# Optimization experiments

Measured on AMD Instinct MI355X. Metric: run time of the kernel, lower is better.

## Reference

```python
import jax, jax.numpy as jnp
import numpy as np

DIM = 1024
HEAD_DIM = 64
CHUNK = 128
B, T = 4, 4096


def setup_inputs() -> dict:
    key = jax.random.key(0)
    ks = jax.random.split(key, 8)
    s = 1.0 / np.sqrt(DIM)
    inp = {
        'x': jax.random.normal(ks[0], (B, T, DIM), jnp.float32),
        'Wq': jax.random.normal(ks[1], (DIM, DIM), jnp.float32) * s,
        'bq': jnp.zeros((DIM,), jnp.float32),
        'Wk': jax.random.normal(ks[2], (DIM, DIM), jnp.float32) * s,
        'bk': jnp.zeros((DIM,), jnp.float32),
        'Wv': jax.random.normal(ks[3], (DIM, DIM), jnp.float32) * s,
        'bv': jnp.zeros((DIM,), jnp.float32),
        'Wbeta': jax.random.normal(ks[4], (DIM, DIM), jnp.float32) * s,
        'bbeta': jnp.zeros((DIM,), jnp.float32),
        'Walpha': jax.random.normal(ks[5], (DIM, DIM), jnp.float32) * s,
        'balpha': jnp.full((DIM,), 2.0, jnp.float32),  # bias init 2.0 as in torch
    }
    return inp


def reference(x, Wq, bq, Wk, bk, Wv, bv, Wbeta, bbeta, Walpha, balpha):
    Bsz, Tlen, D = x.shape
    d = HEAD_DIM
    H = D // d
    C = CHUNK
    scale = d ** (-0.5)

    q = ((x @ Wq.T + bq) * scale).reshape(Bsz, Tlen, H, d)
    k = ((x @ Wk.T + bk) * scale).reshape(Bsz, Tlen, H, d)
    v = (x @ Wv.T + bv).reshape(Bsz, Tlen, H, d)
    alpha_logits = jnp.clip((x @ Walpha.T + balpha).reshape(Bsz, Tlen, H, d), -10.0, 10.0)
    log_alpha = jax.nn.log_sigmoid(alpha_logits)
    alpha_val = jax.nn.sigmoid(alpha_logits)
    beta = jax.nn.softplus(x @ Wbeta.T + bbeta).reshape(Bsz, Tlen, H, d)

    # pad T to a multiple of C (static)
    pad = (-Tlen) % C
    if pad:
        pw = ((0, 0), (0, pad), (0, 0), (0, 0))
        q, k, v = jnp.pad(q, pw), jnp.pad(k, pw), jnp.pad(v, pw)
        log_alpha, beta = jnp.pad(log_alpha, pw), jnp.pad(beta, pw)
    N = q.shape[1] // C
    cshape = (Bsz, N, C, H, d)
    q, k, v = q.reshape(cshape), k.reshape(cshape), v.reshape(cshape)
    log_alpha, beta = log_alpha.reshape(cshape), beta.reshape(cshape)

    ccum = jnp.cumsum(log_alpha, axis=2)          # (B,N,C,H,d)
    m = ccum.mean(axis=-1)                        # (B,N,C,H); mean is linear -> take before pairwise diff
    decay_logits_mean = m[:, :, :, None, :] - m[:, :, None, :, :]  # (B,N,C,C,H)
    tril = jnp.tril(jnp.ones((C, C), jnp.float32))[None, None, :, :, None]
    decay_logits_mean = jnp.where(tril == 0, -1e9, decay_logits_mean)
    decay = jnp.exp(decay_logits_mean)            # (B,N,C,C,H)

    attn = jnp.einsum('bnihd,bnjhd->bnhij', q, k)
    attn = attn * decay.transpose(0, 1, 4, 2, 3)
    y_intra = jnp.einsum('bnhij,bnjhd->bnihd', attn, v * beta)  # (B,N,C,H,d)

    # inter-chunk recurrence via scan over chunks
    asum = jnp.exp(log_alpha.sum(axis=2).mean(axis=-1))  # (B,N,H) total chunk decay
    curve = jnp.exp(m)                                   # (B,N,C,H) intra-chunk decay curve
    bmean = beta.mean(axis=-1)                           # (B,N,C,H)

    def to_scan(a):
        return jnp.moveaxis(a, 1, 0)
    xs = (to_scan(q), to_scan(y_intra), to_scan(curve), to_scan(asum),
          to_scan(k), to_scan(v), to_scan(bmean))

    state0 = jnp.zeros((Bsz, H, d, d), jnp.float32)

    def step(state, inputs):
        qi, yi, ci, ai, ki, vi, bmi = inputs
        mem = jnp.einsum('bchq,bhqk->bchk', qi, state)
        y = yi + mem * ci[..., None]
        state = state * ai[:, :, None, None]
        delta = jnp.einsum('bchk,bchv,bch->bhkv', ki, vi, bmi)
        return state + delta, y

    state, ys = jax.lax.scan(step, state0, xs)
    y = jnp.moveaxis(ys, 0, 1).reshape(Bsz, N * C, D)
    if pad:
        y = y[:, :Tlen, :]
    return y, state, alpha_val
```

## Files before the change

### kernel.cpp

```cpp
#include <hip/hip_runtime.h>
#include <cstdint>
#include <cmath>

#define DIMM 1024
#define NHEAD 16
#define HEADD 64
#define CHUNKC 128
#define NBATCH 4
#define TLEN 4096
#define NCHUNK 32
#define BT (NBATCH * TLEN)
#define NSTACK (5 * DIMM)

typedef unsigned short ushort_t;
typedef __attribute__((ext_vector_type(8))) short short8;
typedef __attribute__((ext_vector_type(4))) float f32x4;

__device__ __forceinline__ float blo(unsigned int u) { return __uint_as_float(u << 16); }
__device__ __forceinline__ float bhi(unsigned int u) { return __uint_as_float(u & 0xffff0000u); }
__device__ __forceinline__ ushort_t f2bf(float f) {
  unsigned int u = __float_as_uint(f);
  u += 0x7fffu + ((u >> 16) & 1u);
  return (ushort_t)(u >> 16);
}
__device__ __forceinline__ float bf2f(ushort_t s) { return __uint_as_float(((unsigned int)s) << 16); }
__device__ __forceinline__ unsigned pack2(float a, float b) {
  return (unsigned)f2bf(a) | ((unsigned)f2bf(b) << 16);
}

__device__ __forceinline__ void async16(const ushort_t* g, ushort_t* l) {
  __builtin_amdgcn_global_load_lds((__attribute__((address_space(1))) void*)g,
                                   (__attribute__((address_space(3))) void*)l, 16, 0, 0);
}

__global__ __launch_bounds__(256) void k_cast(
    const float* __restrict__ x,
    const float* __restrict__ Wq, const float* __restrict__ Wk,
    const float* __restrict__ Wv, const float* __restrict__ Wb, const float* __restrict__ Wa,
    const float* __restrict__ bq, const float* __restrict__ bk,
    const float* __restrict__ bv, const float* __restrict__ bb, const float* __restrict__ ba,
    ushort_t* __restrict__ xb, ushort_t* __restrict__ wbm, float* __restrict__ bias_st) {
  const long XU = (long)BT * DIMM / 4;
  const long WU = (long)NSTACK * DIMM / 4;
  const long BU = NSTACK / 4;
  const long NU = XU + WU + BU;
  for (long u = (long)blockIdx.x * blockDim.x + threadIdx.x; u < NU;
       u += (long)gridDim.x * blockDim.x) {
    if (u < XU) {
      float4 f = ((const float4*)x)[u];
      ushort4 o;
      o.x = f2bf(f.x); o.y = f2bf(f.y); o.z = f2bf(f.z); o.w = f2bf(f.w);
      ((ushort4*)xb)[u] = o;
    } else if (u < XU + WU) {
      long j = u - XU;
      long e = j * 4;
      int row = (int)(e >> 10);
      int col = (int)(e & 1023);
      int p = row >> 10, wr = row & 1023;
      const float* Wp = (p == 0) ? Wq : (p == 1) ? Wk : (p == 2) ? Wv : (p == 3) ? Wb : Wa;
      float4 f = *(const float4*)(Wp + (size_t)wr * DIMM + col);
      ushort4 o;
      o.x = f2bf(f.x); o.y = f2bf(f.y); o.z = f2bf(f.z); o.w = f2bf(f.w);
      ((ushort4*)wbm)[j] = o;
    } else {
      long j = u - XU - WU;
      int e = (int)(j * 4);
      int p = e >> 10, r = e & 1023;
      const float* bp = (p == 0) ? bq : (p == 1) ? bk : (p == 2) ? bv : (p == 3) ? bb : ba;
      ((float4*)bias_st)[j] = *(const float4*)(bp + r);
    }
  }
}

__global__ __launch_bounds__(256) void k_proj(
    const ushort_t* __restrict__ xb, const ushort_t* __restrict__ wbm,
    const float* __restrict__ bias_st,
    ushort_t* __restrict__ qo, ushort_t* __restrict__ ko,
    ushort_t* __restrict__ vo, ushort_t* __restrict__ bo,
    float* __restrict__ ao) {
  __shared__ ushort_t As[128 * 32];
  __shared__ ushort_t Bs[128 * 32];
  const int tid = threadIdx.x;
  const int bn0 = blockIdx.x * 128;
  const int bm0 = blockIdx.y * 128;
  const int lane = tid & 63;
  const int wave = tid >> 6;
  const int quad = lane >> 4, lr = lane & 15;
  const int wr = (wave >> 1) * 64, wc = (wave & 1) * 64;

  f32x4 zero = {0.f, 0.f, 0.f, 0.f};
  f32x4 acc[4][4];
#pragma unroll
  for (int i = 0; i < 4; ++i)
#pragma unroll
    for (int j = 0; j < 4; ++j) acc[i][j] = zero;

  const int r0 = tid >> 2;
  const int c0 = (tid & 3) * 8;
  const ushort_t* ag0 = xb + (size_t)(bm0 + r0) * DIMM + c0;
  const ushort_t* ag1 = xb + (size_t)(bm0 + r0 + 64) * DIMM + c0;
  const ushort_t* bg0 = wbm + (size_t)(bn0 + r0) * DIMM + c0;
  const ushort_t* bg1 = wbm + (size_t)(bn0 + r0 + 64) * DIMM + c0;
  ushort_t* la0 = As + tid * 8;
  ushort_t* la1 = As + 2048 + tid * 8;
  ushort_t* lb0 = Bs + tid * 8;
  ushort_t* lb1 = Bs + 2048 + tid * 8;

  for (int kk = 0; kk < DIMM; kk += 32) {
    __syncthreads();
    async16(ag0 + kk, la0);
    async16(ag1 + kk, la1);
    async16(bg0 + kk, lb0);
    async16(bg1 + kk, lb1);
    __syncthreads();
    short8 af[4], bfr[4];
#pragma unroll
    for (int i = 0; i < 4; ++i)
      af[i] = *(const short8*)(As + (wr + i * 16 + lr) * 32 + quad * 8);
#pragma unroll
    for (int j = 0; j < 4; ++j)
      bfr[j] = *(const short8*)(Bs + (wc + j * 16 + lr) * 32 + quad * 8);
#pragma unroll
    for (int i = 0; i < 4; ++i)
#pragma unroll
      for (int j = 0; j < 4; ++j)
        acc[i][j] = __builtin_amdgcn_mfma_f32_16x16x32_bf16(af[i], bfr[j], acc[i][j], 0, 0, 0);
  }

  const int p = bn0 >> 10;
  const int ncol0 = bn0 & 1023;
#pragma unroll
  for (int j = 0; j < 4; ++j) {
    const int colg = wc + j * 16 + lr;
    const float bias = bias_st[bn0 + colg];
    const int nc = ncol0 + colg;
#pragma unroll
    for (int i = 0; i < 4; ++i) {
#pragma unroll
      for (int r = 0; r < 4; ++r) {
        const int rowl = wr + i * 16 + quad * 4 + r;
        const size_t o = (size_t)(bm0 + rowl) * DIMM + nc;
        float val = acc[i][j][r] + bias;
        if (p == 0) {
          qo[o] = f2bf(val * 0.125f);
        } else if (p == 1) {
          ko[o] = f2bf(val * 0.125f);
        } else if (p == 2) {
          vo[o] = f2bf(val);
        } else if (p == 3) {
          float sp = (val > 20.f) ? val : log1pf(expf(val));
          bo[o] = f2bf(sp);
        } else {
          float c = fminf(fmaxf(val, -10.f), 10.f);
          ao[o] = 1.f / (1.f + expf(-c));
        }
      }
    }
  }
}

__global__ __launch_bounds__(128) void k_stats(
    const float* __restrict__ alpha, const ushort_t* __restrict__ betaw,
    float* __restrict__ mArr, float* __restrict__ bmean, float* __restrict__ asum) {
  const int bnh = blockIdx.x;
  const int h = bnh & 15, n = (bnh >> 4) & 31, b = bnh >> 9;
  const int c = threadIdx.x;
  const size_t bt = (size_t)b * TLEN + n * CHUNKC + c;

  const float4* ap = (const float4*)(alpha + bt * DIMM + h * HEADD);
  float ls = 0.f;
#pragma unroll
  for (int w = 0; w < 16; ++w) {
    float4 a = ap[w];
    ls += logf(a.x) + logf(a.y) + logf(a.z) + logf(a.w);
  }
  const uint4* bp = (const uint4*)(betaw + bt * DIMM + h * HEADD);
  float bs = 0.f;
#pragma unroll
  for (int w = 0; w < 8; ++w) {
    uint4 u = bp[w];
    bs += blo(u.x) + bhi(u.x) + blo(u.y) + bhi(u.y) + blo(u.z) + bhi(u.z) + blo(u.w) + bhi(u.w);
  }
  float la = ls * (1.f / 64.f);

  __shared__ float s[128];
  s[c] = la;
  __syncthreads();
  for (int off = 1; off < 128; off <<= 1) {
    float t = (c >= off) ? s[c - off] : 0.f;
    __syncthreads();
    s[c] += t;
    __syncthreads();
  }
  float m = s[c];
  const size_t o = (size_t)bnh * CHUNKC + c;
  mArr[o] = m;
  bmean[o] = bs * (1.f / 64.f);
  if (c == 127) asum[bnh] = expf(m);
}

__global__ __launch_bounds__(256) void k_delta(
    const ushort_t* __restrict__ kw, const ushort_t* __restrict__ vw,
    const float* __restrict__ bmean, float* __restrict__ delta) {
  __shared__ ushort_t kc[8192];
  __shared__ ushort_t vc[8192];
  __shared__ float bm[128];
  const int bnh = blockIdx.x;
  const int h = bnh & 15, n = (bnh >> 4) & 31, b = bnh >> 9;
  const int tid = threadIdx.x;
  const size_t bt0 = (size_t)b * TLEN + n * CHUNKC;

#pragma unroll
  for (int it = 0; it < 4; ++it) {
    int u = tid + it * 256;
    int row = u >> 3, col = (u & 7) * 8;
    size_t go = (bt0 + row) * DIMM + h * HEADD + col;
    ((uint4*)kc)[u] = *(const uint4*)(kw + go);
    ((uint4*)vc)[u] = *(const uint4*)(vw + go);
  }
  if (tid < 128) bm[tid] = bmean[(size_t)bnh * CHUNKC + tid];
  __syncthreads();

  const int kd = tid >> 2, v0 = (tid & 3) * 16;
  float acc[16];
#pragma unroll
  for (int l = 0; l < 16; ++l) acc[l] = 0.f;

#pragma unroll 4
  for (int c = 0; c < 128; ++c) {
    float kb = bf2f(kc[c * 64 + kd]) * bm[c];
    const uint4* vr = (const uint4*)(vc + c * 64 + v0);
    uint4 u0 = vr[0], u1 = vr[1];
    acc[0] += kb * blo(u0.x);  acc[1] += kb * bhi(u0.x);
    acc[2] += kb * blo(u0.y);  acc[3] += kb * bhi(u0.y);
    acc[4] += kb * blo(u0.z);  acc[5] += kb * bhi(u0.z);
    acc[6] += kb * blo(u0.w);  acc[7] += kb * bhi(u0.w);
    acc[8] += kb * blo(u1.x);  acc[9] += kb * bhi(u1.x);
    acc[10] += kb * blo(u1.y); acc[11] += kb * bhi(u1.y);
    acc[12] += kb * blo(u1.z); acc[13] += kb * bhi(u1.z);
    acc[14] += kb * blo(u1.w); acc[15] += kb * bhi(u1.w);
  }
  float* dst = delta + (size_t)bnh * 4096 + kd * 64 + v0;
#pragma unroll
  for (int l4 = 0; l4 < 4; ++l4)
    ((float4*)dst)[l4] = make_float4(acc[l4 * 4], acc[l4 * 4 + 1], acc[l4 * 4 + 2], acc[l4 * 4 + 3]);
}

__global__ __launch_bounds__(256) void k_scan(
    const float* __restrict__ delta, const float* __restrict__ asum,
    float* __restrict__ Earr, float* __restrict__ state_out) {
  const int bh = blockIdx.x >> 4;
  const int g = blockIdx.x & 15;
  const int b = bh >> 4, h = bh & 15;
  const int elem = g * 256 + threadIdx.x;
  float e = 0.f;
  for (int n = 0; n < 32; ++n) {
    const size_t o = (((size_t)b * 32 + n) * 16 + h) * 4096 + elem;
    const float a = asum[((size_t)b * 32 + n) * 16 + h];
    Earr[o] = e;
    e = e * a + delta[o];
  }
  state_out[(size_t)bh * 4096 + elem] = e;
}

__global__ __launch_bounds__(256) void k_y(
    const ushort_t* __restrict__ qw, const ushort_t* __restrict__ kw,
    const ushort_t* __restrict__ vw, const ushort_t* __restrict__ betaw,
    const float* __restrict__ mArr, const float* __restrict__ Earr,
    float* __restrict__ yout) {
  __shared__ __align__(16) ushort_t vbt[64][200];
  __shared__ __align__(16) ushort_t pst[4][32][40];
  __shared__ float ms[128];
  const int bnh = blockIdx.x;
  const int h = bnh & 15, n = (bnh >> 4) & 31, b = bnh >> 9;
  const int tid = threadIdx.x;
  const int lane = tid & 63;
  const int wv = tid >> 6;
  const int quad = lane >> 4, lr = lane & 15;
  const int i0 = wv * 32;
  const size_t bt0 = (size_t)b * TLEN + n * CHUNKC;
  const size_t hoff = (size_t)h * HEADD;

#pragma unroll
  for (int it = 0; it < 4; ++it) {
    int u = tid + it * 256;
    int j = u & 127, vd0 = (u >> 7) * 8;
    size_t go = (bt0 + j) * DIMM + hoff + vd0;
    uint4 vv = *(const uint4*)(vw + go);
    uint4 bb2 = *(const uint4*)(betaw + go);
    vbt[vd0 + 0][j] = f2bf(blo(vv.x) * blo(bb2.x));
    vbt[vd0 + 1][j] = f2bf(bhi(vv.x) * bhi(bb2.x));
    vbt[vd0 + 2][j] = f2bf(blo(vv.y) * blo(bb2.y));
    vbt[vd0 + 3][j] = f2bf(bhi(vv.y) * bhi(bb2.y));
    vbt[vd0 + 4][j] = f2bf(blo(vv.z) * blo(bb2.z));
    vbt[vd0 + 5][j] = f2bf(bhi(vv.z) * bhi(bb2.z));
    vbt[vd0 + 6][j] = f2bf(blo(vv.w) * blo(bb2.w));
    vbt[vd0 + 7][j] = f2bf(bhi(vv.w) * bhi(bb2.w));
  }
  const float4* Eg = (const float4*)(Earr + (size_t)bnh * 4096);
#pragma unroll
  for (int it = 0; it < 4; ++it) {
    int u = tid + it * 256;
    int kd = u >> 4, vd0 = (u & 15) * 4;
    float4 ev = Eg[u];
    vbt[vd0 + 0][128 + kd] = f2bf(ev.x);
    vbt[vd0 + 1][128 + kd] = f2bf(ev.y);
    vbt[vd0 + 2][128 + kd] = f2bf(ev.z);
    vbt[vd0 + 3][128 + kd] = f2bf(ev.w);
  }
  if (tid < 128) ms[tid] = mArr[(size_t)bnh * CHUNKC + tid];
  __syncthreads();

  short8 qa[2][2];
#pragma unroll
  for (int it = 0; it < 2; ++it) {
    const ushort_t* qg = qw + (bt0 + i0 + it * 16 + lr) * DIMM + hoff + quad * 8;
    qa[it][0] = *(const short8*)(qg);
    qa[it][1] = *(const short8*)(qg + 32);
  }
  float mi[2][4];
#pragma unroll
  for (int it = 0; it < 2; ++it)
#pragma unroll
    for (int r = 0; r < 4; ++r) mi[it][r] = ms[i0 + it * 16 + quad * 4 + r];

  f32x4 zero = {0.f, 0.f, 0.f, 0.f};
  f32x4 acc2[2][4];
#pragma unroll
  for (int it = 0; it < 2; ++it)
#pragma unroll
    for (int nt = 0; nt < 4; ++nt) acc2[it][nt] = zero;

  for (int js = 0; js < 4; ++js) {
    const int j0 = js * 32;
#pragma unroll
    for (int jsub = 0; jsub < 2; ++jsub) {
      const int j0s = j0 + jsub * 16;
      const ushort_t* kg = kw + (bt0 + j0s + lr) * DIMM + hoff + quad * 8;
      short8 kb0 = *(const short8*)(kg);
      short8 kb1 = *(const short8*)(kg + 32);
      const float mj = ms[j0s + lr];
#pragma unroll
      for (int it = 0; it < 2; ++it) {
        f32x4 s = __builtin_amdgcn_mfma_f32_16x16x32_bf16(qa[it][0], kb0, zero, 0, 0, 0);
        s = __builtin_amdgcn_mfma_f32_16x16x32_bf16(qa[it][1], kb1, s, 0, 0, 0);
#pragma unroll
        for (int r = 0; r < 4; ++r) {
          const int ig = i0 + it * 16 + quad * 4 + r;
          const int jg = j0s + lr;
          float w = (jg > ig) ? 0.f : s[r] * __expf(mi[it][r] - mj);
          pst[wv][it * 16 + quad * 4 + r][jsub * 16 + lr] = f2bf(w);
        }
      }
    }
#pragma unroll
    for (int it = 0; it < 2; ++it) {
      short8 pa = *(const short8*)&pst[wv][it * 16 + lr][quad * 8];
#pragma unroll
      for (int nt = 0; nt < 4; ++nt) {
        short8 vb = *(const short8*)&vbt[nt * 16 + lr][j0 + quad * 8];
        acc2[it][nt] = __builtin_amdgcn_mfma_f32_16x16x32_bf16(pa, vb, acc2[it][nt], 0, 0, 0);
      }
    }
  }

#pragma unroll
  for (int es = 0; es < 2; ++es) {
    const int kd0 = es * 32;
    {
      const int row = lane >> 1;
      const int col0 = (lane & 1) * 16;
      const float ex = __expf(ms[i0 + row]);
      const ushort_t* qg = qw + (bt0 + i0 + row) * DIMM + hoff + kd0 + col0;
      uint4 u0 = *(const uint4*)(qg);
      uint4 u1 = *(const uint4*)(qg + 8);
      uint4 w0, w1;
      w0.x = pack2(blo(u0.x) * ex, bhi(u0.x) * ex);
      w0.y = pack2(blo(u0.y) * ex, bhi(u0.y) * ex);
      w0.z = pack2(blo(u0.z) * ex, bhi(u0.z) * ex);
      w0.w = pack2(blo(u0.w) * ex, bhi(u0.w) * ex);
      w1.x = pack2(blo(u1.x) * ex, bhi(u1.x) * ex);
      w1.y = pack2(blo(u1.y) * ex, bhi(u1.y) * ex);
      w1.z = pack2(blo(u1.z) * ex, bhi(u1.z) * ex);
      w1.w = pack2(blo(u1.w) * ex, bhi(u1.w) * ex);
      *(uint4*)&pst[wv][row][col0] = w0;
      *(uint4*)&pst[wv][row][col0 + 8] = w1;
    }
#pragma unroll
    for (int it = 0; it < 2; ++it) {
      short8 pa = *(const short8*)&pst[wv][it * 16 + lr][quad * 8];
#pragma unroll
      for (int nt = 0; nt < 4; ++nt) {
        short8 vb = *(const short8*)&vbt[nt * 16 + lr][128 + kd0 + quad * 8];
        acc2[it][nt] = __builtin_amdgcn_mfma_f32_16x16x32_bf16(pa, vb, acc2[it][nt], 0, 0, 0);
      }
    }
  }

#pragma unroll
  for (int it = 0; it < 2; ++it) {
#pragma unroll
    for (int nt = 0; nt < 4; ++nt) {
      f32x4 a = acc2[it][nt];
#pragma unroll
      for (int r = 0; r < 4; ++r) {
        const int ig = i0 + it * 16 + quad * 4 + r;
        yout[(bt0 + ig) * DIMM + hoff + nt * 16 + lr] = a[r];
      }
    }
  }
}

extern "C" void kernel_launch(void* const* d_in, const int* in_sizes, int n_in,
                              void* d_out, int out_size, void* d_ws, size_t ws_size,
                              hipStream_t stream) {
  const float* x  = (const float*)d_in[0];
  const float* Wq = (const float*)d_in[1];
  const float* bq = (const float*)d_in[2];
  const float* Wk = (const float*)d_in[3];
  const float* bk = (const float*)d_in[4];
  const float* Wv = (const float*)d_in[5];
  const float* bv = (const float*)d_in[6];
  const float* Wb = (const float*)d_in[7];
  const float* bb = (const float*)d_in[8];
  const float* Wa = (const float*)d_in[9];
  const float* ba = (const float*)d_in[10];

  char* ws = (char*)d_ws;
  ushort_t* xb   = (ushort_t*)(ws + 0);
  ushort_t* wbm  = (ushort_t*)(ws + 33554432);
  float* bias_st = (float*)(ws + 44040192);
  ushort_t* qw   = (ushort_t*)(ws + 44060672);
  ushort_t* kw   = (ushort_t*)(ws + 77615104);
  ushort_t* vw   = (ushort_t*)(ws + 111169536);
  ushort_t* bw   = (ushort_t*)(ws + 144723968);
  float* mArr    = (float*)(ws + 178278400);
  float* bmean   = (float*)(ws + 179326976);
  float* asum    = (float*)(ws + 180375552);
  float* delta   = (float*)(ws + 180383744);
  float* Earr    = (float*)(ws + 213938176);

  float* yout = (float*)d_out;
  float* state_out = yout + (size_t)BT * DIMM;
  float* aout = state_out + (size_t)NBATCH * NHEAD * 64 * 64;

  k_cast<<<dim3(4096), dim3(256), 0, stream>>>(x, Wq, Wk, Wv, Wb, Wa,
                                               bq, bk, bv, bb, ba, xb, wbm, bias_st);
  k_proj<<<dim3(40, 128), dim3(256), 0, stream>>>(xb, wbm, bias_st, qw, kw, vw, bw, aout);
  k_stats<<<dim3(2048), dim3(128), 0, stream>>>(aout, bw, mArr, bmean, asum);
  k_delta<<<dim3(2048), dim3(256), 0, stream>>>(kw, vw, bmean, delta);
  k_scan<<<dim3(1024), dim3(256), 0, stream>>>(delta, asum, Earr, state_out);
  k_y<<<dim3(2048), dim3(256), 0, stream>>>(qw, kw, vw, bw, mArr, Earr, yout);
}
```

Measured before the change: 661.4 us.

## Rewrite projection GEMM as 256x256 double-buffered ping-pong MFMA pipeline

The fused 5-way projection GEMM moves from 128x128 tiles with K=32 and a full sync per step to 256x256 tiles with K=64, 512 threads and 128KB of double-buffered LDS. Loads are XOR-swizzled to avoid bank conflicts, and async global-to-LDS copies are interleaved with quadrant MFMA blocks using setprio and vmcnt waits. The block index is remapped so neighbouring blocks share tiles in L2. This targets low MFMA utilisation and exposed load latency in the dominant GEMM, but raises register and LDS pressure, and the hand-scheduled barrier ordering is fragile.

Measured after the change: 743.3 us. +12.4%, slower.

```diff
diff --git a/kernel.cpp b/kernel.cpp
--- a/kernel.cpp
+++ b/kernel.cpp
@@ -72,92 +72,149 @@
   }
 }
 
-__global__ __launch_bounds__(256) void k_proj(
+#define REGN(bb,op,hh) ((((bb)*2+(op))*2+(hh))*16384)
+
+#define STAGE(bb,op,hh,kt) do {                                                   \
+    const ushort_t* _g = ((op) ? wbm + (((size_t)(bn0 + (hh)*128 + srow)) << 10)  \
+                               : xb  + (((size_t)(bm0 + (hh)*128 + srow)) << 10)) \
+                          + (kt)*64 + sswz;                                       \
+    char* _l = sm + REGN(bb,op,hh) + tid*16;                                      \
+    async16(_g, (ushort_t*)_l);                                                   \
+    async16(_g + (64 << 10), (ushort_t*)(_l + 8192));                             \
+  } while(0)
+
+#define LDA(bb,Qr) do {                                                           \
+    const char* _b = sm + REGN(bb,0,Qr) + ((wm*64 + lr) << 7);                    \
+    _Pragma("unroll") for (int _f = 0; _f < 4; ++_f) {                            \
+      a_[_f][0] = *(const short8*)(_b + (_f<<11) + (((0|quad)^sx)<<4));           \
+      a_[_f][1] = *(const short8*)(_b + (_f<<11) + (((4|quad)^sx)<<4));           \
+    } } while(0)
+
+#define LDB(bb,Qc) do {                                                           \
+    const char* _b = sm + REGN(bb,1,Qc) + ((wn*32 + lr) << 7);                    \
+    _Pragma("unroll") for (int _g = 0; _g < 2; ++_g) {                            \
+      b_[Qc][_g][0] = *(const short8*)(_b + (_g<<11) + (((0|quad)^sx)<<4));       \
+      b_[Qc][_g][1] = *(const short8*)(_b + (_g<<11) + (((4|quad)^sx)<<4));       \
+    } } while(0)
+
+#define MFMAQ(Qr,Qc) do {                                                         \
+    __builtin_amdgcn_s_setprio(1);                                                \
+    _Pragma("unroll") for (int _f = 0; _f < 4; ++_f)                              \
+    _Pragma("unroll") for (int _g = 0; _g < 2; ++_g) {                            \
+      acc[Qr][Qc][_f][_g] = __builtin_amdgcn_mfma_f32_16x16x32_bf16(              \
+          a_[_f][0], b_[Qc][_g][0], acc[Qr][Qc][_f][_g], 0, 0, 0);                \
+      acc[Qr][Qc][_f][_g] = __builtin_amdgcn_mfma_f32_16x16x32_bf16(              \
+          a_[_f][1], b_[Qc][_g][1], acc[Qr][Qc][_f][_g], 0, 0, 0);                \
+    }                                                                             \
+    __builtin_amdgcn_s_setprio(0); } while(0)
+
+#define BARR __builtin_amdgcn_s_barrier()
+#define VMC(n) asm volatile("s_waitcnt vmcnt(" #n ")" ::: "memory")
+
+__global__ __launch_bounds__(512, 2) void k_proj(
     const ushort_t* __restrict__ xb, const ushort_t* __restrict__ wbm,
     const float* __restrict__ bias_st,
     ushort_t* __restrict__ qo, ushort_t* __restrict__ ko,
     ushort_t* __restrict__ vo, ushort_t* __restrict__ bo,
     float* __restrict__ ao) {
-  __shared__ ushort_t As[128 * 32];
-  __shared__ ushort_t Bs[128 * 32];
+  __shared__ __align__(16) char sm[131072];
   const int tid = threadIdx.x;
-  const int bn0 = blockIdx.x * 128;
-  const int bm0 = blockIdx.y * 128;
   const int lane = tid & 63;
-  const int wave = tid >> 6;
+  const int wv = tid >> 6;
+  const int wm = wv >> 2;
+  const int wn = wv & 3;
   const int quad = lane >> 4, lr = lane & 15;
-  const int wr = (wave >> 1) * 64, wc = (wave & 1) * 64;
+  const int sx = lr & 7;
+
+  const int id = blockIdx.x;
+  const int swz = (id & 7) * 160 + (id >> 3);
+  const int by = swz / 20;
+  const int bx = swz - by * 20;
+  const int bm0 = by * 256, bn0 = bx * 256;
+
+  const int srow = tid >> 3;
+  const int sswz = ((tid & 7) ^ (srow & 7)) << 3;
 
   f32x4 zero = {0.f, 0.f, 0.f, 0.f};
-  f32x4 acc[4][4];
-#pragma unroll
-  for (int i = 0; i < 4; ++i)
-#pragma unroll
-    for (int j = 0; j < 4; ++j) acc[i][j] = zero;
-
-  const int r0 = tid >> 2;
-  const int c0 = (tid & 3) * 8;
-  const ushort_t* ag0 = xb + (size_t)(bm0 + r0) * DIMM + c0;
-  const ushort_t* ag1 = xb + (size_t)(bm0 + r0 + 64) * DIMM + c0;
-  const ushort_t* bg0 = wbm + (size_t)(bn0 + r0) * DIMM + c0;
-  const ushort_t* bg1 = wbm + (size_t)(bn0 + r0 + 64) * DIMM + c0;
-  ushort_t* la0 = As + tid * 8;
-  ushort_t* la1 = As + 2048 + tid * 8;
-  ushort_t* lb0 = Bs + tid * 8;
-  ushort_t* lb1 = Bs + 2048 + tid * 8;
-
-  for (int kk = 0; kk < DIMM; kk += 32) {
-    __syncthreads();
-    async16(ag0 + kk, la0);
-    async16(ag1 + kk, la1);
-    async16(bg0 + kk, lb0);
-    async16(bg1 + kk, lb1);
-    __syncthreads();
-    short8 af[4], bfr[4];
-#pragma unroll
-    for (int i = 0; i < 4; ++i)
-      af[i] = *(const short8*)(As + (wr + i * 16 + lr) * 32 + quad * 8);
-#pragma unroll
-    for (int j = 0; j < 4; ++j)
-      bfr[j] = *(const short8*)(Bs + (wc + j * 16 + lr) * 32 + quad * 8);
-#pragma unroll
-    for (int i = 0; i < 4; ++i)
-#pragma unroll
-      for (int j = 0; j < 4; ++j)
-        acc[i][j] = __builtin_amdgcn_mfma_f32_16x16x32_bf16(af[i], bfr[j], acc[i][j], 0, 0, 0);
-  }
-
-  const int p = bn0 >> 10;
+  f32x4 acc[2][2][4][2];
+#pragma unroll
+  for (int i = 0; i < 2; ++i)
+#pragma unroll
+    for (int j = 0; j < 2; ++j)
+#pragma unroll
+      for (int f = 0; f < 4; ++f)
+#pragma unroll
+        for (int g = 0; g < 2; ++g) acc[i][j][f][g] = zero;
+
+  short8 a_[4][2];
+  short8 b_[2][2][2];
+
+  STAGE(0,0,0,0); STAGE(0,0,1,0); STAGE(0,1,0,0); STAGE(0,1,1,0);
+  STAGE(1,0,0,1); STAGE(1,0,1,1); STAGE(1,1,0,1); STAGE(1,1,1,1);
+  VMC(8);
+  BARR;
+
+#pragma unroll 1
+  for (int t2 = 0; t2 < 8; ++t2) {
+    const int te = 2 * t2;
+    const bool enA = (t2 > 0);
+    const bool enB = (t2 < 7);
+    LDA(0,0); LDB(0,0); if (enA) STAGE(1,1,0, te+1); BARR; MFMAQ(0,0); BARR;
+    LDB(0,1);           if (enA) STAGE(1,0,0, te+1); BARR; MFMAQ(0,1); BARR;
+    LDA(0,1);           if (enB) STAGE(0,0,0, te+2); BARR; MFMAQ(1,0); BARR;
+                        if (enB) STAGE(0,1,0, te+2); BARR; MFMAQ(1,1);
+    if (t2 == 7) { VMC(0); } else { VMC(4); }
+    BARR;
+    const bool enC = (t2 < 7);
+    LDA(1,1); LDB(1,1); if (enC) STAGE(0,1,1, te+2); BARR; MFMAQ(1,1); BARR;
+    LDB(1,0);           if (enC) STAGE(0,0,1, te+2); BARR; MFMAQ(1,0); BARR;
+    LDA(1,0);           if (enC) STAGE(1,0,1, te+3); BARR; MFMAQ(0,1); BARR;
+                        if (enC) STAGE(1,1,1, te+3); BARR; MFMAQ(0,0);
+    if (t2 < 7) { VMC(4); BARR; }
+  }
+
+  const int p_id = bn0 >> 10;
   const int ncol0 = bn0 & 1023;
 #pragma unroll
-  for (int j = 0; j < 4; ++j) {
-    const int colg = wc + j * 16 + lr;
-    const float bias = bias_st[bn0 + colg];
-    const int nc = ncol0 + colg;
-#pragma unroll
-    for (int i = 0; i < 4; ++i) {
-#pragma unroll
-      for (int r = 0; r < 4; ++r) {
-        const int rowl = wr + i * 16 + quad * 4 + r;
-        const size_t o = (size_t)(bm0 + rowl) * DIMM + nc;
-        float val = acc[i][j][r] + bias;
-        if (p == 0) {
-          qo[o] = f2bf(val * 0.125f);
-        } else if (p == 1) {
-          ko[o] = f2bf(val * 0.125f);
-        } else if (p == 2) {
-          vo[o] = f2bf(val);
-        } else if (p == 3) {
-          float sp = (val > 20.f) ? val : log1pf(expf(val));
-          bo[o] = f2bf(sp);
-        } else {
-          float c = fminf(fmaxf(val, -10.f), 10.f);
-          ao[o] = 1.f / (1.f + expf(-c));
-        }
-      }
-    }
-  }
-}
+  for (int Qc = 0; Qc < 2; ++Qc)
+#pragma unroll
+    for (int g = 0; g < 2; ++g) {
+      const int colg = Qc * 128 + wn * 32 + g * 16 + lr;
+      const float bias = bias_st[bn0 + colg];
+      const int nc = ncol0 + colg;
+#pragma unroll
+      for (int Qr = 0; Qr < 2; ++Qr)
+#pragma unroll
+        for (int f = 0; f < 4; ++f)
+#pragma unroll
+          for (int r = 0; r < 4; ++r) {
+            const int rowl = Qr * 128 + wm * 64 + f * 16 + quad * 4 + r;
+            const size_t o = (size_t)(bm0 + rowl) * DIMM + nc;
+            float val = acc[Qr][Qc][f][g][r] + bias;
+            if (p_id == 0) {
+              qo[o] = f2bf(val * 0.125f);
+            } else if (p_id == 1) {
+              ko[o] = f2bf(val * 0.125f);
+            } else if (p_id == 2) {
+              vo[o] = f2bf(val);
+            } else if (p_id == 3) {
+              float sp = (val > 20.f) ? val : log1pf(expf(val));
+              bo[o] = f2bf(sp);
+            } else {
+              float c = fminf(fmaxf(val, -10.f), 10.f);
+              ao[o] = 1.f / (1.f + expf(-c));
+            }
+          }
+    }
+}
+
+#undef REGN
+#undef STAGE
+#undef LDA
+#undef LDB
+#undef MFMAQ
+#undef BARR
+#undef VMC
 
 __global__ __launch_bounds__(128) void k_stats(
     const float* __restrict__ alpha, const ushort_t* __restrict__ betaw,
@@ -446,7 +503,7 @@
 
   k_cast<<<dim3(4096), dim3(256), 0, stream>>>(x, Wq, Wk, Wv, Wb, Wa,
                                                bq, bk, bv, bb, ba, xb, wbm, bias_st);
-  k_proj<<<dim3(40, 128), dim3(256), 0, stream>>>(xb, wbm, bias_st, qw, kw, vw, bw, aout);
+  k_proj<<<dim3(1280), dim3(512), 0, stream>>>(xb, wbm, bias_st, qw, kw, vw, bw, aout);
   k_stats<<<dim3(2048), dim3(128), 0, stream>>>(aout, bw, mArr, bmean, asum);
   k_delta<<<dim3(2048), dim3(256), 0, stream>>>(kw, vw, bmean, delta);
   k_scan<<<dim3(1024), dim3(256), 0, stream>>>(delta, asum, Earr, state_out);
```

## Widen projection GEMM K-tile, swizzle LDS, remap blocks, stage bf16 stores through LDS

Applied to the files above, without the earlier changes.

The projection GEMM now loads 64-wide K slices per iteration, which halves the number of barrier pairs. It stores tiles in LDS with an XOR swizzle to avoid bank conflicts on fragment reads. Block indices are remapped in groups of eight for better L2 reuse of input and weight tiles. The bf16 outputs are transposed through shared memory so each thread writes 16-byte vector stores instead of scattered 2-byte stores. The cost is more LDS per block (64 KB), which may lower occupancy, plus extra barriers in the epilogue.

After: 677.6 us. 1.02x slower.

```diff
diff --git a/kernel.cpp b/kernel.cpp
--- a/kernel.cpp
+++ b/kernel.cpp
@@ -78,15 +78,26 @@
     ushort_t* __restrict__ qo, ushort_t* __restrict__ ko,
     ushort_t* __restrict__ vo, ushort_t* __restrict__ bo,
     float* __restrict__ ao) {
-  __shared__ ushort_t As[128 * 32];
-  __shared__ ushort_t Bs[128 * 32];
+  __shared__ __align__(16) ushort_t smem[2 * 128 * 64];
+  ushort_t* As = smem;
+  ushort_t* Bs = smem + 128 * 64;
   const int tid = threadIdx.x;
-  const int bn0 = blockIdx.x * 128;
-  const int bm0 = blockIdx.y * 128;
   const int lane = tid & 63;
   const int wave = tid >> 6;
   const int quad = lane >> 4, lr = lane & 15;
   const int wr = (wave >> 1) * 64, wc = (wave & 1) * 64;
+  const int sx = lr & 7;
+
+  const int lid = blockIdx.y * 40 + blockIdx.x;
+  const int swz = (lid & 7) * 640 + (lid >> 3);
+  const int byn = swz / 40;
+  const int bxn = swz - byn * 40;
+  const int bm0 = byn * 128, bn0 = bxn * 128;
+
+  const int trow = tid >> 3;
+  const int gsw = ((tid & 7) ^ (trow & 7)) << 3;
+  const ushort_t* agb = xb + (size_t)(bm0 + trow) * DIMM + gsw;
+  const ushort_t* bgb = wbm + (size_t)(bn0 + trow) * DIMM + gsw;
 
   f32x4 zero = {0.f, 0.f, 0.f, 0.f};
   f32x4 acc[4][4];
@@ -95,66 +106,84 @@
 #pragma unroll
     for (int j = 0; j < 4; ++j) acc[i][j] = zero;
 
-  const int r0 = tid >> 2;
-  const int c0 = (tid & 3) * 8;
-  const ushort_t* ag0 = xb + (size_t)(bm0 + r0) * DIMM + c0;
-  const ushort_t* ag1 = xb + (size_t)(bm0 + r0 + 64) * DIMM + c0;
-  const ushort_t* bg0 = wbm + (size_t)(bn0 + r0) * DIMM + c0;
-  const ushort_t* bg1 = wbm + (size_t)(bn0 + r0 + 64) * DIMM + c0;
-  ushort_t* la0 = As + tid * 8;
-  ushort_t* la1 = As + 2048 + tid * 8;
-  ushort_t* lb0 = Bs + tid * 8;
-  ushort_t* lb1 = Bs + 2048 + tid * 8;
-
-  for (int kk = 0; kk < DIMM; kk += 32) {
+  for (int kk = 0; kk < DIMM; kk += 64) {
     __syncthreads();
-    async16(ag0 + kk, la0);
-    async16(ag1 + kk, la1);
-    async16(bg0 + kk, lb0);
-    async16(bg1 + kk, lb1);
+#pragma unroll
+    for (int c = 0; c < 4; ++c) {
+      async16(agb + (size_t)(c * 32) * DIMM + kk, As + c * 2048 + tid * 8);
+      async16(bgb + (size_t)(c * 32) * DIMM + kk, Bs + c * 2048 + tid * 8);
+    }
     __syncthreads();
-    short8 af[4], bfr[4];
-#pragma unroll
-    for (int i = 0; i < 4; ++i)
-      af[i] = *(const short8*)(As + (wr + i * 16 + lr) * 32 + quad * 8);
-#pragma unroll
-    for (int j = 0; j < 4; ++j)
-      bfr[j] = *(const short8*)(Bs + (wc + j * 16 + lr) * 32 + quad * 8);
-#pragma unroll
-    for (int i = 0; i < 4; ++i)
+#pragma unroll
+    for (int kh = 0; kh < 2; ++kh) {
+      short8 af[4], bfr[4];
+#pragma unroll
+      for (int i = 0; i < 4; ++i)
+        af[i] = *(const short8*)(As + (wr + i * 16 + lr) * 64 + (((kh * 4 + quad) ^ sx) << 3));
 #pragma unroll
       for (int j = 0; j < 4; ++j)
-        acc[i][j] = __builtin_amdgcn_mfma_f32_16x16x32_bf16(af[i], bfr[j], acc[i][j], 0, 0, 0);
-  }
-
-  const int p = bn0 >> 10;
+        bfr[j] = *(const short8*)(Bs + (wc + j * 16 + lr) * 64 + (((kh * 4 + quad) ^ sx) << 3));
+#pragma unroll
+      for (int i = 0; i < 4; ++i)
+#pragma unroll
+        for (int j = 0; j < 4; ++j)
+          acc[i][j] = __builtin_amdgcn_mfma_f32_16x16x32_bf16(af[i], bfr[j], acc[i][j], 0, 0, 0);
+    }
+  }
+
+  const int p_id = bn0 >> 10;
   const int ncol0 = bn0 & 1023;
-#pragma unroll
-  for (int j = 0; j < 4; ++j) {
-    const int colg = wc + j * 16 + lr;
-    const float bias = bias_st[bn0 + colg];
-    const int nc = ncol0 + colg;
-#pragma unroll
-    for (int i = 0; i < 4; ++i) {
-#pragma unroll
-      for (int r = 0; r < 4; ++r) {
-        const int rowl = wr + i * 16 + quad * 4 + r;
-        const size_t o = (size_t)(bm0 + rowl) * DIMM + nc;
-        float val = acc[i][j][r] + bias;
-        if (p == 0) {
-          qo[o] = f2bf(val * 0.125f);
-        } else if (p == 1) {
-          ko[o] = f2bf(val * 0.125f);
-        } else if (p == 2) {
-          vo[o] = f2bf(val);
-        } else if (p == 3) {
-          float sp = (val > 20.f) ? val : log1pf(expf(val));
-          bo[o] = f2bf(sp);
-        } else {
+
+  if (p_id == 4) {
+#pragma unroll
+    for (int j = 0; j < 4; ++j) {
+      const int colg = wc + j * 16 + lr;
+      const float bias = bias_st[bn0 + colg];
+      const int nc = ncol0 + colg;
+#pragma unroll
+      for (int i = 0; i < 4; ++i)
+#pragma unroll
+        for (int r = 0; r < 4; ++r) {
+          const int rowl = wr + i * 16 + quad * 4 + r;
+          float val = acc[i][j][r] + bias;
           float c = fminf(fmaxf(val, -10.f), 10.f);
-          ao[o] = 1.f / (1.f + expf(-c));
+          ao[(size_t)(bm0 + rowl) * DIMM + nc] = 1.f / (1.f + expf(-c));
+        }
+    }
+  } else {
+    ushort_t* outp = (p_id == 0) ? qo : (p_id == 1) ? ko : (p_id == 2) ? vo : bo;
+    const float scl = (p_id <= 1) ? 0.125f : 1.f;
+    ushort_t* T = smem;
+    const int halfb = (wr == 64) ? 32 : 0;
+#pragma unroll
+    for (int pass = 0; pass < 2; ++pass) {
+      __syncthreads();
+#pragma unroll
+      for (int ii = 0; ii < 2; ++ii) {
+        const int i = pass * 2 + ii;
+#pragma unroll
+        for (int j = 0; j < 4; ++j) {
+          const int col = wc + j * 16 + lr;
+          const float bias = bias_st[bn0 + col];
+#pragma unroll
+          for (int r = 0; r < 4; ++r) {
+            float val = acc[i][j][r] + bias;
+            float ov;
+            if (p_id == 3) ov = (val > 20.f) ? val : log1pf(expf(val));
+            else ov = val * scl;
+            T[(halfb + ii * 16 + quad * 4 + r) * 136 + col] = f2bf(ov);
+          }
         }
       }
+      __syncthreads();
+      const int trw = tid >> 2;
+      const int cch = (tid & 3) * 32;
+      const int growl = pass * 32 + (trw & 31) + (trw >> 5) * 64;
+      ushort_t* dst = outp + (size_t)(bm0 + growl) * DIMM + ncol0 + cch;
+      const ushort_t* src = T + trw * 136 + cch;
+#pragma unroll
+      for (int u = 0; u < 4; ++u)
+        *(uint4*)(dst + u * 8) = *(const uint4*)(src + u * 8);
     }
   }
 }
```
